# Kernel tuning notes

Measured on AMD Instinct MI355X. Metric: run time of the kernel, lower is better.

## Reference

```python
import jax, jax.numpy as jnp
from jax import lax
import numpy as np

KS = 8        # window size
SS = 4        # shift size = KS // 2
HEADS = 4


def _l2n(t, axis):
    # torch F.normalize: x / clamp(||x||_2, min=eps)
    return t / jnp.maximum(jnp.linalg.norm(t, axis=axis, keepdims=True), 1e-12)


def _to_windows(t, heads, ks):
    # 'b (head c) (h kh) (w kw) -> b head (h w) (kh kw) c'
    b, hc, H, W = t.shape
    c = hc // heads
    hW, wW = H // ks, W // ks
    t = t.reshape(b, heads, c, hW, ks, wW, ks)
    t = t.transpose(0, 1, 3, 5, 4, 6, 2)  # b,h,hW,wW,kh,kw,c
    return t.reshape(b, heads, hW * wW, ks * ks, c)


def _from_windows(t, hW, wW, ks):
    # 'b head (h w) (kh kw) c -> b (head c) (h kh) (w kw)'
    b, heads, nW, kk, c = t.shape
    t = t.reshape(b, heads, hW, wW, ks, ks, c)
    t = t.transpose(0, 1, 6, 2, 4, 3, 5)  # b,h,c,hW,kh,wW,kw
    return t.reshape(b, heads * c, hW * ks, wW * ks)


def _talk_conv(attn, w, hW, wW):
    # Conv3d(heads->heads, kernel (3,3,1), padding same) over the (hW, wW, K)
    # grid; kernel size 1 on K means an independent 2D conv per K slot, so we
    # fold K into the batch dim and run a single 2D conv.
    b, heads, nW, a1, a2 = attn.shape
    K = a1 * a2
    t = attn.reshape(b, heads, hW, wW, K).transpose(0, 4, 1, 2, 3)
    t = t.reshape(b * K, heads, hW, wW)
    t = lax.conv_general_dilated(t, w, (1, 1), 'SAME',
                                 dimension_numbers=('NCHW', 'OIHW', 'NCHW'))
    t = t.reshape(b, K, heads, hW, wW).transpose(0, 2, 3, 4, 1)
    return t.reshape(b, heads, nW, a1, a2)


def _shift_mask(H, W, ks, ss):
    # Swin-style shifted-window mask; pure numpy constant (shapes are static).
    img = np.zeros((H, W), np.float32)
    cnt = 0
    for hs in (slice(0, -ks), slice(-ks, -ss), slice(-ss, None)):
        for ws in (slice(0, -ks), slice(-ks, -ss), slice(-ss, None)):
            img[hs, ws] = cnt
            cnt += 1
    win = img.reshape(H // ks, ks, W // ks, ks).transpose(0, 2, 1, 3).reshape(-1, ks * ks)
    diff = win[:, None, :] - win[:, :, None]
    return jnp.asarray(np.where(diff != 0, -100.0, 0.0).astype(np.float32))


def _forward(x, w_quz, w_kv, temperature, r_talking, g_talking,
             b_talking_w, l_talking_w, dw_u_w, project_w, project_out_w,
             sca_w, sca_b):
    b, c, H, W = x.shape
    hW, wW = H // KS, W // KS
    quz = jnp.einsum('oc,bchw->bohw', w_quz, x)
    q, u, z = jnp.split(quz, 3, axis=1)
    kv = jnp.einsum('oc,bchw->bohw', w_kv, x)
    k, v = jnp.split(kv, 2, axis=1)
    # shift = True
    q, k, v = (jnp.roll(t, (-SS, -SS), axis=(-1, -2)) for t in (q, k, v))
    q, k, v = (_to_windows(t, HEADS, KS) for t in (q, k, v))  # b,h,nW,kk,c
    qb, ql, qg, qr = jnp.split(q, 4, axis=-1)
    kb, kl, kg, kr = jnp.split(k, 4, axis=-1)
    vb, vl, vg, vr = jnp.split(v, 4, axis=-1)
    qb, kb = _l2n(qb, -1), _l2n(kb, -1)
    ql, kl = _l2n(ql, -2), _l2n(kl, -2)
    qg, kg = _l2n(qg, -3), _l2n(kg, -3)
    qr, kr = _l2n(qr, -3), _l2n(kr, -3)
    # 4 branches (n=window index, i/j=position-in-window, c/d=per-branch chan)
    attn_b = jnp.einsum('bhnic,bhnjc->bhnij', qb, kb) * temperature[0]
    attn_l = jnp.einsum('bhnic,bhnid->bhncd', ql, kl) * temperature[1]
    attn_g = jnp.einsum('bhnic,bhnid->bhicd', qg, kg) * temperature[2]
    attn_r = jnp.einsum('bhnic,bhnjc->bhcij', qr, kr) * temperature[3]
    # talking heads
    attn_b = _talk_conv(attn_b, b_talking_w, hW, wW)
    attn_l = _talk_conv(attn_l, l_talking_w, hW, wW)
    attn_g = jnp.einsum('hklt,bhkcd->btlcd', g_talking, attn_g)
    attn_r = jnp.einsum('hcdt,bhcij->btdij', r_talking, attn_r)
    # shifted-window mask on the brightness branch
    attn_b = attn_b + _shift_mask(H, W, KS, SS)[None, None]
    attn_b, attn_l, attn_g, attn_r = (jax.nn.softmax(t, axis=-1)
                                      for t in (attn_b, attn_l, attn_g, attn_r))
    # outputs, all arranged to (b,h,n,i,c) before un-windowing
    out_b = jnp.einsum('bhnij,bhnjc->bhnic', attn_b, vb)
    out_l = jnp.einsum('bhncd,bhnid->bhnic', attn_l, vl)
    out_g = jnp.einsum('bhicd,bhnid->bhnic', attn_g, vg)
    out_r = jnp.einsum('bhcij,bhnjc->bhnic', attn_r, vr)
    out = jnp.concatenate([_from_windows(t, hW, wW, KS)
                           for t in (out_b, out_l, out_g, out_r)], axis=1)
    out = jnp.roll(out, (SS, SS), axis=(-1, -2))
    # simplified channel attention (global avg pool + 1x1 conv with bias)
    s = jnp.mean(out, axis=(2, 3))
    s = jnp.einsum('oc,bc->bo', sca_w, s) + sca_b
    out = jnp.einsum('oc,bchw->bohw', project_w, out * s[:, :, None, None])
    dw = lax.conv_general_dilated(u, dw_u_w, (1, 1), 'SAME',
                                  feature_group_count=u.shape[1],
                                  dimension_numbers=('NCHW', 'OIHW', 'NCHW'))
    out = out + dw
    return jnp.einsum('oc,bchw->bohw', project_out_w, out * z)


def setup_inputs() -> dict:
    key = jax.random.key(0)
    ks = jax.random.split(key, 12)
    dim, h_dim = 64, 128
    cd = h_dim // HEADS // 4
    b, H, W = 4, 192, 192
    r = lambda i, shp, s: jax.random.normal(ks[i], shp, jnp.float32) * s
    return {
        'x': jax.random.normal(ks[0], (b, dim, H, W), jnp.float32),
        'w_quz': r(1, (3 * h_dim, dim), 0.1),
        'w_kv': r(2, (2 * h_dim, dim), 0.1),
        'temperature': jnp.ones((4, HEADS, 1, 1, 1), jnp.float32),
        'r_talking': r(3, (HEADS, cd, cd, HEADS), 0.2),
        'g_talking': r(4, (HEADS, KS * KS, KS * KS, HEADS), 0.05),
        'b_talking_w': r(5, (HEADS, HEADS, 3, 3), 0.2),
        'l_talking_w': r(6, (HEADS, HEADS, 3, 3), 0.2),
        'dw_u_w': r(7, (h_dim, 1, 3, 3), 0.2),
        'project_w': r(8, (h_dim, h_dim), 0.08),
        'project_out_w': r(9, (dim, h_dim), 0.08),
        'sca_w': r(10, (h_dim, h_dim), 0.08),
        'sca_b': jnp.zeros((h_dim,), jnp.float32),
    }


def reference(x, w_quz, w_kv, temperature, r_talking, g_talking,
              b_talking_w, l_talking_w, dw_u_w, project_w, project_out_w,
              sca_w, sca_b):
    return _forward(x, w_quz, w_kv, temperature, r_talking, g_talking,
                    b_talking_w, l_talking_w, dw_u_w, project_w,
                    project_out_w, sca_w, sca_b)
```

## Files before the change

kernel.cpp:

```cpp
#include <hip/hip_runtime.h>
#include <cstdint>
#include <cstddef>

#define BB   4
#define CIN  64
#define HD   128
#define NH   4
#define CHW  32
#define CB   8
#define IMG  192
#define SSH  4
#define NWS  24
#define NWIN 576
#define KK   64
#define HWP  (IMG*IMG)

static const size_t NQK16  = (size_t)NH*NWIN*KK*16;
static const size_t NV32   = (size_t)NH*NWIN*KK*CHW;
static const size_t NGR    = (size_t)NH*KK*NWIN*CB;
static const size_t NSP    = (size_t)HD*HWP;
static const size_t NATTNB = (size_t)NH*NWIN*KK*KK;
static const size_t NATTNL = (size_t)NH*NWIN*64;
static const size_t NATTNG = (size_t)NH*KK*64;
static const size_t NATTNR = (size_t)NH*CB*KK*KK;
static const size_t NPART  = (size_t)8*NATTNR;

__device__ inline float wave_max(float v){
  #pragma unroll
  for (int s=1;s<64;s<<=1) v = fmaxf(v, __shfl_xor(v, s));
  return v;
}
__device__ inline float wave_sum(float v){
  #pragma unroll
  for (int s=1;s<64;s<<=1) v += __shfl_xor(v, s);
  return v;
}
__device__ inline float g8_max(float v){
  v = fmaxf(v, __shfl_xor(v,1)); v = fmaxf(v, __shfl_xor(v,2)); v = fmaxf(v, __shfl_xor(v,4));
  return v;
}
__device__ inline float g8_sum(float v){
  v += __shfl_xor(v,1); v += __shfl_xor(v,2); v += __shfl_xor(v,4);
  return v;
}
__device__ inline int regionc(int y){ return (y < IMG-8) ? 0 : ((y < IMG-4) ? 1 : 2); }

__device__ inline size_t widx(int h,int n,int i,int c){
  return (((size_t)h*NWIN + n)*KK + i)*CHW + c;
}
__device__ inline size_t widx16(int h,int n,int i,int c){
  return (((size_t)h*NWIN + n)*KK + i)*16 + c;
}
__device__ inline size_t gidx(int h,int i,int n,int c){
  return (((size_t)(h*KK + i))*NWIN + n)*CB + c;
}
__device__ inline size_t ridx(int h,int c,int n,int i){
  return (((size_t)(h*CB + c))*NWIN + n)*KK + i;
}

__global__ __launch_bounds__(256) void k1_proj(
    const float* __restrict__ x, const float* __restrict__ wquz, const float* __restrict__ wkv,
    float* __restrict__ qw, float* __restrict__ kw, float* __restrict__ vw,
    float* __restrict__ qg, float* __restrict__ kg,
    float* __restrict__ qr, float* __restrict__ kr,
    float* __restrict__ u, float* __restrict__ zbuf, int bsel)
{
  __shared__ float xs[64][16];
  int blk = blockIdx.x;
  int xc = blk % 12, y = blk / 12;
  int x0 = xc*16;
  int t = threadIdx.x;
  {
    int c = t >> 2, p4 = (t & 3)*4;
    float4 v = *(const float4*)&x[((size_t)(bsel*CIN+c)*IMG + y)*IMG + x0 + p4];
    *(float4*)&xs[c][p4] = v;
  }
  int py  = (y + IMG - SSH) % IMG;
  int kh  = py & 7, hwq = py >> 3;
  int wwA = ((x0 - SSH + IMG) % IMG) >> 3;
  int wwB = x0 >> 3;
  int wwC = (x0 + 8) >> 3;
  int pnA = hwq*NWS + wwA, pnB = hwq*NWS + wwB, pnC = hwq*NWS + wwC;
  int piA = kh*8 + 4, piB = kh*8, piC = kh*8;
  #define PN_(p) ((p)<4 ? pnA : ((p)<12 ? pnB : pnC))
  #define PI_(p) ((p)<4 ? (piA+(p)) : ((p)<12 ? (piB+(p)-4) : (piC+(p)-12)))
  __syncthreads();

  bool qkz = (t < 128);
  const float* wr1 = wquz + (size_t)t*CIN;
  const float* wr2 = wkv  + (size_t)t*CIN;

  float acc1[16], acc2[16], acc3[16];
  #pragma unroll
  for (int p = 0; p < 16; ++p){ acc1[p]=0.f; acc2[p]=0.f; acc3[p]=0.f; }

  if (qkz){
    const float* wr3 = wquz + (size_t)(t+256)*CIN;
    for (int cc4 = 0; cc4 < 64; cc4 += 4){
      float4 w1 = *(const float4*)(wr1+cc4);
      float4 w2 = *(const float4*)(wr2+cc4);
      float4 w3 = *(const float4*)(wr3+cc4);
      float w1a[4]={w1.x,w1.y,w1.z,w1.w};
      float w2a[4]={w2.x,w2.y,w2.z,w2.w};
      float w3a[4]={w3.x,w3.y,w3.z,w3.w};
      #pragma unroll
      for (int j = 0; j < 4; ++j){
        #pragma unroll
        for (int q = 0; q < 4; ++q){
          float4 xv = *(const float4*)&xs[cc4+j][q*4];
          acc1[q*4+0]+=w1a[j]*xv.x; acc1[q*4+1]+=w1a[j]*xv.y; acc1[q*4+2]+=w1a[j]*xv.z; acc1[q*4+3]+=w1a[j]*xv.w;
          acc2[q*4+0]+=w2a[j]*xv.x; acc2[q*4+1]+=w2a[j]*xv.y; acc2[q*4+2]+=w2a[j]*xv.z; acc2[q*4+3]+=w2a[j]*xv.w;
          acc3[q*4+0]+=w3a[j]*xv.x; acc3[q*4+1]+=w3a[j]*xv.y; acc3[q*4+2]+=w3a[j]*xv.z; acc3[q*4+3]+=w3a[j]*xv.w;
        }
      }
    }
    int h = t >> 5, c = t & 31;
    if (c < 16){
      #pragma unroll
      for (int p = 0; p < 16; ++p) qw[widx16(h,PN_(p),PI_(p),c)] = acc1[p];
      #pragma unroll
      for (int p = 0; p < 16; ++p) kw[widx16(h,PN_(p),PI_(p),c)] = acc2[p];
    } else if (c < 24){
      int cg = c - 16;
      #pragma unroll
      for (int p = 0; p < 16; ++p) qg[gidx(h,PI_(p),PN_(p),cg)] = acc1[p];
      #pragma unroll
      for (int p = 0; p < 16; ++p) kg[gidx(h,PI_(p),PN_(p),cg)] = acc2[p];
    } else {
      int cr = c - 24;
      *(float4*)&qr[ridx(h,cr,pnA,piA)]   = make_float4(acc1[0],acc1[1],acc1[2],acc1[3]);
      *(float4*)&qr[ridx(h,cr,pnB,piB)]   = make_float4(acc1[4],acc1[5],acc1[6],acc1[7]);
      *(float4*)&qr[ridx(h,cr,pnB,piB+4)] = make_float4(acc1[8],acc1[9],acc1[10],acc1[11]);
      *(float4*)&qr[ridx(h,cr,pnC,piC)]   = make_float4(acc1[12],acc1[13],acc1[14],acc1[15]);
      *(float4*)&kr[ridx(h,cr,pnA,piA)]   = make_float4(acc2[0],acc2[1],acc2[2],acc2[3]);
      *(float4*)&kr[ridx(h,cr,pnB,piB)]   = make_float4(acc2[4],acc2[5],acc2[6],acc2[7]);
      *(float4*)&kr[ridx(h,cr,pnB,piB+4)] = make_float4(acc2[8],acc2[9],acc2[10],acc2[11]);
      *(float4*)&kr[ridx(h,cr,pnC,piC)]   = make_float4(acc2[12],acc2[13],acc2[14],acc2[15]);
    }
    size_t zb = ((size_t)t*IMG + y)*IMG + x0;
    *(float4*)&zbuf[zb+ 0] = make_float4(acc3[0],acc3[1],acc3[2],acc3[3]);
    *(float4*)&zbuf[zb+ 4] = make_float4(acc3[4],acc3[5],acc3[6],acc3[7]);
    *(float4*)&zbuf[zb+ 8] = make_float4(acc3[8],acc3[9],acc3[10],acc3[11]);
    *(float4*)&zbuf[zb+12] = make_float4(acc3[12],acc3[13],acc3[14],acc3[15]);
  } else {
    for (int cc4 = 0; cc4 < 64; cc4 += 4){
      float4 w1 = *(const float4*)(wr1+cc4);
      float4 w2 = *(const float4*)(wr2+cc4);
      float w1a[4]={w1.x,w1.y,w1.z,w1.w};
      float w2a[4]={w2.x,w2.y,w2.z,w2.w};
      #pragma unroll
      for (int j = 0; j < 4; ++j){
        #pragma unroll
        for (int q = 0; q < 4; ++q){
          float4 xv = *(const float4*)&xs[cc4+j][q*4];
          acc1[q*4+0]+=w1a[j]*xv.x; acc1[q*4+1]+=w1a[j]*xv.y; acc1[q*4+2]+=w1a[j]*xv.z; acc1[q*4+3]+=w1a[j]*xv.w;
          acc2[q*4+0]+=w2a[j]*xv.x; acc2[q*4+1]+=w2a[j]*xv.y; acc2[q*4+2]+=w2a[j]*xv.z; acc2[q*4+3]+=w2a[j]*xv.w;
        }
      }
    }
    int ch = t - 128;
    size_t ub = ((size_t)ch*IMG + y)*IMG + x0;
    *(float4*)&u[ub+ 0] = make_float4(acc1[0],acc1[1],acc1[2],acc1[3]);
    *(float4*)&u[ub+ 4] = make_float4(acc1[4],acc1[5],acc1[6],acc1[7]);
    *(float4*)&u[ub+ 8] = make_float4(acc1[8],acc1[9],acc1[10],acc1[11]);
    *(float4*)&u[ub+12] = make_float4(acc1[12],acc1[13],acc1[14],acc1[15]);
    int h = ch >> 5, c = ch & 31;
    #pragma unroll
    for (int p = 0; p < 16; ++p) vw[widx(h,PN_(p),PI_(p),c)] = acc2[p];
  }
  #undef PN_
  #undef PI_
}

__global__ __launch_bounds__(256) void kA(
    const float* __restrict__ qw, const float* __restrict__ kw,
    const float* __restrict__ qg, const float* __restrict__ kg,
    const float* __restrict__ qr, const float* __restrict__ kr,
    const float* __restrict__ temp,
    float* __restrict__ attnB, float* __restrict__ attnL,
    float* __restrict__ attnG, float* __restrict__ part,
    float* __restrict__ invqr, float* __restrict__ invkr)
{
  __shared__ __align__(16) char smem[36864];
  int blk = blockIdx.x;
  int t = threadIdx.x;

  if (blk < 576){
    float (*qs)[64][8] = (float(*)[64][8])smem;
    int wv = t >> 6, j = t & 63;
    int gid = blk*4 + wv;
    int n = gid % NWIN, h = gid / NWIN;
    size_t base = widx16(h,n,j,0);
    float q8[CB], k8[CB];
    float sq = 0.f, sk2 = 0.f;
    #pragma unroll
    for (int c = 0; c < CB; ++c){
      q8[c] = qw[base+c]; sq += q8[c]*q8[c];
      k8[c] = kw[base+c]; sk2 += k8[c]*k8[c];
    }
    float invq = 1.f/fmaxf(sqrtf(sq),1e-12f), invk = 1.f/fmaxf(sqrtf(sk2),1e-12f);
    #pragma unroll
    for (int c = 0; c < CB; ++c){ qs[wv][j][c] = q8[c]*invq; k8[c] *= invk; }
    __syncthreads();
    float tmp = temp[h];
    float* orow = attnB + (size_t)gid*KK*KK;
    for (int i = 0; i < KK; ++i){
      float a = 0.f;
      #pragma unroll
      for (int c = 0; c < CB; ++c) a += qs[wv][i][c]*k8[c];
      orow[(size_t)i*KK + j] = a * tmp;
    }
  } else if (blk < 1152){
    int b2 = blk - 576;
    float (*qs)[64][8] = (float(*)[64][8])smem;
    float (*ks)[64][8] = (float(*)[64][8])(smem + 8192);
    float (*invqA)[8] = (float(*)[8])(smem + 16384);
    float (*invkA)[8] = (float(*)[8])(smem + 16384 + 128);
    int wv = t >> 6, tl = t & 63;
    int gid = b2*4 + wv;
    int n = gid % NWIN, h = gid / NWIN;
    size_t base = widx16(h,n,tl,8);
    #pragma unroll
    for (int c = 0; c < CB; ++c){ qs[wv][tl][c] = qw[base+c]; ks[wv][tl][c] = kw[base+c]; }
    __syncthreads();
    int c8 = tl & 7, ig = tl >> 3;
    float sq = 0.f, sk2 = 0.f;
    for (int i = ig; i < KK; i += 8){
      float a = qs[wv][i][c8]; sq += a*a;
      float b = ks[wv][i][c8]; sk2 += b*b;
    }
    #pragma unroll
    for (int m = 8; m < 64; m <<= 1){ sq += __shfl_xor(sq,m); sk2 += __shfl_xor(sk2,m); }
    if (tl < 8){ invqA[wv][tl] = 1.f/fmaxf(sqrtf(sq),1e-12f); invkA[wv][tl] = 1.f/fmaxf(sqrtf(sk2),1e-12f); }
    __syncthreads();
    int c = tl >> 3, d = tl & 7;
    float a = 0.f;
    for (int i = 0; i < KK; ++i) a += qs[wv][i][c]*ks[wv][i][d];
    attnL[(size_t)gid*64 + tl] = a * invqA[wv][c] * invkA[wv][d] * temp[NH + h];
  } else if (blk < 1408){
    int b2 = blk - 1152;
    int i = b2 & 63, h = b2 >> 6;
    float* sq = (float*)smem;
    float* sk = sq + 512;
    float (*redA)[64] = (float(*)[64])(smem + 4096);
    float (*redQ)[64] = (float(*)[64])(smem + 4096 + 1024);
    float (*redK)[64] = (float(*)[64])(smem + 4096 + 2048);
    size_t base = ((size_t)(h*KK+i))*NWIN*CB;
    int np = t >> 6, cd = t & 63, c = cd >> 3, d = cd & 7;
    float a = 0.f, qs2 = 0.f, ks2 = 0.f;
    for (int n0 = 0; n0 < NWIN; n0 += 64){
      __syncthreads();
      for (int idx = t; idx < 512; idx += 256){
        sq[idx] = qg[base + (size_t)n0*CB + idx];
        sk[idx] = kg[base + (size_t)n0*CB + idx];
      }
      __syncthreads();
      for (int nn = np; nn < 64; nn += 4){
        float qv = sq[nn*8+c], kv = sk[nn*8+d];
        a += qv*kv; qs2 += qv*qv; ks2 += kv*kv;
      }
    }
    __syncthreads();
    redA[np][cd] = a; redQ[np][cd] = qs2; redK[np][cd] = ks2;
    __syncthreads();
    if (t < 64){
      float at = redA[0][t]+redA[1][t]+redA[2][t]+redA[3][t];
      float qt = redQ[0][t]+redQ[1][t]+redQ[2][t]+redQ[3][t];
      float kt = redK[0][t]+redK[1][t]+redK[2][t]+redK[3][t];
      at *= (1.f/fmaxf(sqrtf(qt),1e-12f)) * (1.f/fmaxf(sqrtf(kt),1e-12f)) * temp[2*NH + h];
      attnG[(size_t)(h*KK+i)*64 + t] = at;
    }
  } else if (blk < 1664){
    int b2 = blk - 1408;
    int chunk = b2 >> 5, hc = b2 & 31;
    int n0 = chunk*72;
    float* sq = (float*)smem;
    float* sk = sq + 72*64;
    size_t base = (size_t)hc*NWIN*KK + (size_t)n0*KK;
    for (int idx = t; idx < 72*64/4; idx += 256){
      *(float4*)&sq[idx*4] = *(const float4*)&qr[base + (size_t)idx*4];
      *(float4*)&sk[idx*4] = *(const float4*)&kr[base + (size_t)idx*4];
    }
    __syncthreads();
    int j = t & 63, ig = t >> 6;
    float acc[16];
    #pragma unroll
    for (int p = 0; p < 16; ++p) acc[p] = 0.f;
    for (int nn = 0; nn < 72; ++nn){
      float kv = sk[nn*64+j];
      #pragma unroll
      for (int p = 0; p < 16; ++p) acc[p] += sq[nn*64 + ig*16 + p]*kv;
    }
    float* ob = part + (size_t)b2*4096;
    #pragma unroll
    for (int p = 0; p < 16; ++p) ob[(size_t)(ig*16+p)*64 + j] = acc[p];
  } else {
    int hc = blk - 1664;
    float (*rq)[64] = (float(*)[64])smem;
    float (*rk)[64] = (float(*)[64])(smem + 1024);
    size_t base = (size_t)hc*NWIN*KK;
    int i = t & 63, ng = t >> 6;
    float sq = 0.f, sk2 = 0.f;
    for (int n = ng; n < NWIN; n += 4){
      float a = qr[base + (size_t)n*KK + i]; sq  += a*a;
      float b = kr[base + (size_t)n*KK + i]; sk2 += b*b;
    }
    rq[ng][i] = sq; rk[ng][i] = sk2;
    __syncthreads();
    if (t < 64){
      float s = rq[0][t]+rq[1][t]+rq[2][t]+rq[3][t];
      invqr[hc*KK + t] = 1.f/fmaxf(sqrtf(s),1e-12f);
    } else if (t < 128){
      int i2 = t - 64;
      float s = rk[0][i2]+rk[1][i2]+rk[2][i2]+rk[3][i2];
      invkr[hc*KK + i2] = 1.f/fmaxf(sqrtf(s),1e-12f);
    }
  }
}

__global__ __launch_bounds__(256) void kB(
    const float* __restrict__ attnB, const float* __restrict__ btw,
    const float* __restrict__ vw, float* __restrict__ outa,
// ... 262 lines not shown
  __shared__ float red[256];
  red[threadIdx.x] = s; __syncthreads();
  for (int k = 128; k > 0; k >>= 1){
    if (threadIdx.x < k) red[threadIdx.x] += red[threadIdx.x + k];
    __syncthreads();
  }
  if (threadIdx.x == 0) meanb[ch] = red[0] / (float)HWP;
}

#define PADX 68
__global__ __launch_bounds__(256) void k9a(
    const float* __restrict__ outa, const float* __restrict__ meanb,
    const float* __restrict__ scaw, const float* __restrict__ scab,
    const float* __restrict__ projw, const float* __restrict__ dwu,
    const float* __restrict__ zbuf, float* __restrict__ out2z)
{
  __shared__ float WT[128][128];
  __shared__ float xsv[128][PADX];
  __shared__ float sv[128];
  int t = threadIdx.x;
  if (t < 128){
    float s = scab[t];
    const float* srow = scaw + (size_t)t*HD;
    for (int c = 0; c < HD; c += 4){
      float4 w = *(const float4*)&srow[c];
      float4 mm = *(const float4*)&meanb[c];
      s += w.x*mm.x + w.y*mm.y + w.z*mm.z + w.w*mm.w;
    }
    sv[t] = s;
  }
  for (int idx = t; idx < 4096; idx += 256){
    int o = idx & 127; int c4 = (idx >> 7) * 4;
    float4 w = *(const float4*)&projw[(size_t)o*HD + c4];
    WT[c4][o] = w.x; WT[c4+1][o] = w.y; WT[c4+2][o] = w.z; WT[c4+3][o] = w.w;
  }
  int px4 = (t & 15) * 4; int og8 = (t >> 4) * 8;
  for (int tile = 0; tile < 2; ++tile){
    int tid = blockIdx.x * 2 + tile;
    int y = tid / 3, x0 = (tid % 3) * 64;
    size_t sb = (size_t)y*IMG + x0;
    __syncthreads();
    for (int idx = t; idx < 2048; idx += 256){
      int c = idx >> 4; int p4 = (idx & 15) * 4;
      float4 v = *(const float4*)&outa[(size_t)c*HWP + sb + p4];
      float s = sv[c];
      xsv[c][p4] = v.x*s; xsv[c][p4+1] = v.y*s; xsv[c][p4+2] = v.z*s; xsv[c][p4+3] = v.w*s;
    }
    __syncthreads();
    float acc[8][4];
    #pragma unroll
    for (int a = 0; a < 8; ++a){ acc[a][0]=0.f; acc[a][1]=0.f; acc[a][2]=0.f; acc[a][3]=0.f; }
    for (int c = 0; c < 128; ++c){
      float4 xv = *(const float4*)&xsv[c][px4];
      float4 wA = *(const float4*)&WT[c][og8];
      float4 wB = *(const float4*)&WT[c][og8+4];
      float w8[8] = {wA.x,wA.y,wA.z,wA.w,wB.x,wB.y,wB.z,wB.w};
      #pragma unroll
      for (int a = 0; a < 8; ++a){
        acc[a][0] += w8[a]*xv.x; acc[a][1] += w8[a]*xv.y;
        acc[a][2] += w8[a]*xv.z; acc[a][3] += w8[a]*xv.w;
      }
    }
    #pragma unroll
    for (int oo = 0; oo < 8; ++oo){
      int o = og8 + oo;
      size_t off = (size_t)o*HWP + sb + px4;
      float4 d = *(const float4*)&dwu[off];
      float4 z = *(const float4*)&zbuf[off];
      float4 r;
      r.x = (acc[oo][0]+d.x)*z.x; r.y = (acc[oo][1]+d.y)*z.y;
      r.z = (acc[oo][2]+d.z)*z.z; r.w = (acc[oo][3]+d.w)*z.w;
      *(float4*)&out2z[off] = r;
    }
  }
}

__global__ __launch_bounds__(256) void k9b(
    const float* __restrict__ out2z, const float* __restrict__ projow,
    float* __restrict__ dout, int bsel)
{
  __shared__ float WT2[128][64];
  __shared__ float xsv[128][PADX];
  int t = threadIdx.x;
  for (int idx = t; idx < 2048; idx += 256){
    int o = idx & 63; int c4 = (idx >> 6) * 4;
    float4 w = *(const float4*)&projow[(size_t)o*HD + c4];
    WT2[c4][o] = w.x; WT2[c4+1][o] = w.y; WT2[c4+2][o] = w.z; WT2[c4+3][o] = w.w;
  }
  int px4 = (t & 15) * 4; int og4 = (t >> 4) * 4;
  for (int tile = 0; tile < 2; ++tile){
    int tid = blockIdx.x * 2 + tile;
    int y = tid / 3, x0 = (tid % 3) * 64;
    size_t sb = (size_t)y*IMG + x0;
    __syncthreads();
    for (int idx = t; idx < 2048; idx += 256){
      int c = idx >> 4; int p4 = (idx & 15) * 4;
      float4 v = *(const float4*)&out2z[(size_t)c*HWP + sb + p4];
      xsv[c][p4] = v.x; xsv[c][p4+1] = v.y; xsv[c][p4+2] = v.z; xsv[c][p4+3] = v.w;
    }
    __syncthreads();
    float acc[4][4];
    #pragma unroll
    for (int a = 0; a < 4; ++a){ acc[a][0]=0.f; acc[a][1]=0.f; acc[a][2]=0.f; acc[a][3]=0.f; }
    for (int c = 0; c < 128; ++c){
      float4 xv = *(const float4*)&xsv[c][px4];
      float4 w4 = *(const float4*)&WT2[c][og4];
      float w4a[4] = {w4.x,w4.y,w4.z,w4.w};
      #pragma unroll
      for (int a = 0; a < 4; ++a){
        acc[a][0] += w4a[a]*xv.x; acc[a][1] += w4a[a]*xv.y;
        acc[a][2] += w4a[a]*xv.z; acc[a][3] += w4a[a]*xv.w;
      }
    }
    #pragma unroll
    for (int oo = 0; oo < 4; ++oo){
      int o = og4 + oo;
      float4 r; r.x = acc[oo][0]; r.y = acc[oo][1]; r.z = acc[oo][2]; r.w = acc[oo][3];
      *(float4*)&dout[(size_t)(bsel*CIN + o)*HWP + sb + px4] = r;
    }
  }
}

extern "C" void kernel_launch(void* const* d_in, const int* in_sizes, int n_in,
                              void* d_out, int out_size, void* d_ws, size_t ws_size,
                              hipStream_t stream)
{
  const float* x     = (const float*)d_in[0];
  const float* wquz  = (const float*)d_in[1];
  const float* wkv   = (const float*)d_in[2];
  const float* temp  = (const float*)d_in[3];
  const float* rtalk = (const float*)d_in[4];
  const float* gtalk = (const float*)d_in[5];
  const float* btw   = (const float*)d_in[6];
  const float* ltw   = (const float*)d_in[7];
  const float* dww   = (const float*)d_in[8];
  const float* projw = (const float*)d_in[9];
  const float* projow= (const float*)d_in[10];
  const float* scaw  = (const float*)d_in[11];
  const float* scab  = (const float*)d_in[12];
  float* dout = (float*)d_out;

  float* ws = (float*)d_ws;
  float* qw    = ws;
  float* kw    = qw + NQK16;
  float* vw    = kw + NQK16;
  float* qg    = vw + NV32;
  float* kg    = qg + NGR;
  float* qr    = kg + NGR;
  float* kr    = qr + NGR;
  float* u     = kr + NGR;
  float* zbuf  = u + NSP;
  float* outa  = zbuf + NSP;
  float* attnB = outa + NSP;
  float* dwu   = attnB;
  float* out2z = attnB + NSP;
  float* attnL = attnB + NATTNB;
  float* attnG = attnL + NATTNL;
  float* attnGp= attnG + NATTNG;
  float* part  = attnGp + NATTNG;
  float* attnR = part + NPART;
  float* attnRp= attnR + NATTNR;
  float* invqr = attnRp + NATTNR;
  float* invkr = invqr + 2048;
  float* meanb = invkr + 2048;

  for (int b = 0; b < BB; ++b){
    k1_proj<<<IMG*12, 256, 0, stream>>>(x, wquz, wkv, qw, kw, vw, qg, kg, qr, kr, u, zbuf, b);

    kA<<<1696, 256, 0, stream>>>(qw, kw, qg, kg, qr, kr, temp,
                                 attnB, attnL, attnG, part, invqr, invkr);

    kB<<<16512, 256, 0, stream>>>(attnB, btw, vw, outa, attnL, ltw,
                                  attnG, gtalk, attnGp, part, invqr, invkr, temp, attnR,
                                  u, dww, out2z );

    kC<<<2336, 256, 0, stream>>>(attnGp, vw, outa, attnR, rtalk, attnRp);

    k7c<<<NH*NWIN, 256, 0, stream>>>(attnRp, vw, outa);

    k8_mean<<<HD, 256, 0, stream>>>(outa, meanb);

    k9a<<<288, 256, 0, stream>>>(outa, meanb, scaw, scab, projw, out2z , zbuf, dwu );
    k9b<<<288, 256, 0, stream>>>(dwu , projow, dout, b);
  }
}
```

Measured before the change: 1.471 ms.

## Rebalance projection kernel so every thread computes all five channel outputs

The projection kernel now processes 32-pixel rows per block. The two thread halves split the pixels, and each thread computes all five weight rows (q, k, z, u, v) for one channel over 16 pixels. Before, threads were split into uneven groups of three and two outputs. This removes warp divergence and load imbalance and halves the grid size, at the cost of more registers per thread (80 accumulators). Workspace aliasing for the dwu and out2z buffers is also remapped: kB's depthwise output moves into the qw region and the k9a/k9b argument roles are swapped.

```diff
diff --git a/kernel.cpp b/kernel.cpp
--- a/kernel.cpp
+++ b/kernel.cpp
@@ -65,109 +65,103 @@
     float* __restrict__ qr, float* __restrict__ kr,
     float* __restrict__ u, float* __restrict__ zbuf, int bsel)
 {
-  __shared__ float xs[64][16];
+  __shared__ float xs[64][32];
   int blk = blockIdx.x;
-  int xc = blk % 12, y = blk / 12;
-  int x0 = xc*16;
+  int xc = blk % 6, y = blk / 6;
+  int x0 = xc*32;
   int t = threadIdx.x;
   {
-    int c = t >> 2, p4 = (t & 3)*4;
-    float4 v = *(const float4*)&x[((size_t)(bsel*CIN+c)*IMG + y)*IMG + x0 + p4];
-    *(float4*)&xs[c][p4] = v;
-  }
+    int c = t >> 2, p8 = (t & 3)*8;
+    const float* xr = &x[((size_t)(bsel*CIN+c)*IMG + y)*IMG + x0 + p8];
+    *(float4*)&xs[c][p8]   = *(const float4*)xr;
+    *(float4*)&xs[c][p8+4] = *(const float4*)(xr+4);
+  }
+  int half = t >> 7, cp = t & 127;
+  int x0h = x0 + half*16;
   int py  = (y + IMG - SSH) % IMG;
   int kh  = py & 7, hwq = py >> 3;
-  int wwA = ((x0 - SSH + IMG) % IMG) >> 3;
-  int wwB = x0 >> 3;
-  int wwC = (x0 + 8) >> 3;
+  int wwA = ((x0h - SSH + IMG) % IMG) >> 3;
+  int wwB = x0h >> 3;
+  int wwC = (x0h + 8) >> 3;
   int pnA = hwq*NWS + wwA, pnB = hwq*NWS + wwB, pnC = hwq*NWS + wwC;
   int piA = kh*8 + 4, piB = kh*8, piC = kh*8;
   #define PN_(p) ((p)<4 ? pnA : ((p)<12 ? pnB : pnC))
   #define PI_(p) ((p)<4 ? (piA+(p)) : ((p)<12 ? (piB+(p)-4) : (piC+(p)-12)))
   __syncthreads();
 
-  bool qkz = (t < 128);
-  const float* wr1 = wquz + (size_t)t*CIN;
-  const float* wr2 = wkv  + (size_t)t*CIN;
-
-  float acc1[16], acc2[16], acc3[16];
+  const float* w0 = wquz + (size_t)cp*CIN;
+  const float* w1 = wkv  + (size_t)cp*CIN;
+  const float* w2 = wquz + (size_t)(cp+256)*CIN;
+  const float* w3 = wquz + (size_t)(cp+128)*CIN;
+  const float* w4 = wkv  + (size_t)(cp+128)*CIN;
+
+  float a0[16], a1[16], a2[16], a3[16], a4[16];
   #pragma unroll
-  for (int p = 0; p < 16; ++p){ acc1[p]=0.f; acc2[p]=0.f; acc3[p]=0.f; }
-
-  if (qkz){
-    const float* wr3 = wquz + (size_t)(t+256)*CIN;
-    for (int cc4 = 0; cc4 < 64; cc4 += 4){
-      float4 w1 = *(const float4*)(wr1+cc4);
-      float4 w2 = *(const float4*)(wr2+cc4);
-      float4 w3 = *(const float4*)(wr3+cc4);
-      float w1a[4]={w1.x,w1.y,w1.z,w1.w};
-      float w2a[4]={w2.x,w2.y,w2.z,w2.w};
-      float w3a[4]={w3.x,w3.y,w3.z,w3.w};
-      #pragma unroll
-      for (int j = 0; j < 4; ++j){
-        #pragma unroll
-        for (int q = 0; q < 4; ++q){
-          float4 xv = *(const float4*)&xs[cc4+j][q*4];
-          acc1[q*4+0]+=w1a[j]*xv.x; acc1[q*4+1]+=w1a[j]*xv.y; acc1[q*4+2]+=w1a[j]*xv.z; acc1[q*4+3]+=w1a[j]*xv.w;
-          acc2[q*4+0]+=w2a[j]*xv.x; acc2[q*4+1]+=w2a[j]*xv.y; acc2[q*4+2]+=w2a[j]*xv.z; acc2[q*4+3]+=w2a[j]*xv.w;
-          acc3[q*4+0]+=w3a[j]*xv.x; acc3[q*4+1]+=w3a[j]*xv.y; acc3[q*4+2]+=w3a[j]*xv.z; acc3[q*4+3]+=w3a[j]*xv.w;
-        }
-      }
-    }
-    int h = t >> 5, c = t & 31;
-    if (c < 16){
-      #pragma unroll
-      for (int p = 0; p < 16; ++p) qw[widx16(h,PN_(p),PI_(p),c)] = acc1[p];
-      #pragma unroll
-      for (int p = 0; p < 16; ++p) kw[widx16(h,PN_(p),PI_(p),c)] = acc2[p];
-    } else if (c < 24){
-      int cg = c - 16;
-      #pragma unroll
-      for (int p = 0; p < 16; ++p) qg[gidx(h,PI_(p),PN_(p),cg)] = acc1[p];
-      #pragma unroll
-      for (int p = 0; p < 16; ++p) kg[gidx(h,PI_(p),PN_(p),cg)] = acc2[p];
-    } else {
-      int cr = c - 24;
-      *(float4*)&qr[ridx(h,cr,pnA,piA)]   = make_float4(acc1[0],acc1[1],acc1[2],acc1[3]);
-      *(float4*)&qr[ridx(h,cr,pnB,piB)]   = make_float4(acc1[4],acc1[5],acc1[6],acc1[7]);
-      *(float4*)&qr[ridx(h,cr,pnB,piB+4)] = make_float4(acc1[8],acc1[9],acc1[10],acc1[11]);
-      *(float4*)&qr[ridx(h,cr,pnC,piC)]   = make_float4(acc1[12],acc1[13],acc1[14],acc1[15]);
-      *(float4*)&kr[ridx(h,cr,pnA,piA)]   = make_float4(acc2[0],acc2[1],acc2[2],acc2[3]);
-      *(float4*)&kr[ridx(h,cr,pnB,piB)]   = make_float4(acc2[4],acc2[5],acc2[6],acc2[7]);
-      *(float4*)&kr[ridx(h,cr,pnB,piB+4)] = make_float4(acc2[8],acc2[9],acc2[10],acc2[11]);
-      *(float4*)&kr[ridx(h,cr,pnC,piC)]   = make_float4(acc2[12],acc2[13],acc2[14],acc2[15]);
-    }
-    size_t zb = ((size_t)t*IMG + y)*IMG + x0;
-    *(float4*)&zbuf[zb+ 0] = make_float4(acc3[0],acc3[1],acc3[2],acc3[3]);
-    *(float4*)&zbuf[zb+ 4] = make_float4(acc3[4],acc3[5],acc3[6],acc3[7]);
-    *(float4*)&zbuf[zb+ 8] = make_float4(acc3[8],acc3[9],acc3[10],acc3[11]);
-    *(float4*)&zbuf[zb+12] = make_float4(acc3[12],acc3[13],acc3[14],acc3[15]);
+  for (int p = 0; p < 16; ++p){ a0[p]=0.f; a1[p]=0.f; a2[p]=0.f; a3[p]=0.f; a4[p]=0.f; }
+
+  int pb = half*16;
+  for (int cc4 = 0; cc4 < 64; cc4 += 4){
+    float4 W0 = *(const float4*)(w0+cc4);
+    float4 W1 = *(const float4*)(w1+cc4);
+    float4 W2 = *(const float4*)(w2+cc4);
+    float4 W3 = *(const float4*)(w3+cc4);
+    float4 W4 = *(const float4*)(w4+cc4);
+    float w0a[4]={W0.x,W0.y,W0.z,W0.w};
+    float w1a[4]={W1.x,W1.y,W1.z,W1.w};
+    float w2a[4]={W2.x,W2.y,W2.z,W2.w};
+    float w3a[4]={W3.x,W3.y,W3.z,W3.w};
+    float w4a[4]={W4.x,W4.y,W4.z,W4.w};
+    #pragma unroll
+    for (int j = 0; j < 4; ++j){
+      float f0=w0a[j], f1=w1a[j], f2=w2a[j], f3=w3a[j], f4=w4a[j];
+      #pragma unroll
+      for (int q = 0; q < 4; ++q){
+        float4 xv = *(const float4*)&xs[cc4+j][pb + q*4];
+        a0[q*4+0]+=f0*xv.x; a0[q*4+1]+=f0*xv.y; a0[q*4+2]+=f0*xv.z; a0[q*4+3]+=f0*xv.w;
+        a1[q*4+0]+=f1*xv.x; a1[q*4+1]+=f1*xv.y; a1[q*4+2]+=f1*xv.z; a1[q*4+3]+=f1*xv.w;
+        a2[q*4+0]+=f2*xv.x; a2[q*4+1]+=f2*xv.y; a2[q*4+2]+=f2*xv.z; a2[q*4+3]+=f2*xv.w;
+        a3[q*4+0]+=f3*xv.x; a3[q*4+1]+=f3*xv.y; a3[q*4+2]+=f3*xv.z; a3[q*4+3]+=f3*xv.w;
+        a4[q*4+0]+=f4*xv.x; a4[q*4+1]+=f4*xv.y; a4[q*4+2]+=f4*xv.z; a4[q*4+3]+=f4*xv.w;
+      }
+    }
+  }
+
+  int h = cp >> 5, c = cp & 31;
+  if (c < 16){
+    #pragma unroll
+    for (int p = 0; p < 16; ++p) qw[widx16(h,PN_(p),PI_(p),c)] = a0[p];
+    #pragma unroll
+    for (int p = 0; p < 16; ++p) kw[widx16(h,PN_(p),PI_(p),c)] = a1[p];
+  } else if (c < 24){
+    int cg = c - 16;
+    #pragma unroll
+    for (int p = 0; p < 16; ++p) qg[gidx(h,PI_(p),PN_(p),cg)] = a0[p];
+    #pragma unroll
+    for (int p = 0; p < 16; ++p) kg[gidx(h,PI_(p),PN_(p),cg)] = a1[p];
   } else {
-    for (int cc4 = 0; cc4 < 64; cc4 += 4){
-      float4 w1 = *(const float4*)(wr1+cc4);
-      float4 w2 = *(const float4*)(wr2+cc4);
-      float w1a[4]={w1.x,w1.y,w1.z,w1.w};
-      float w2a[4]={w2.x,w2.y,w2.z,w2.w};
-      #pragma unroll
-      for (int j = 0; j < 4; ++j){
-        #pragma unroll
-        for (int q = 0; q < 4; ++q){
-          float4 xv = *(const float4*)&xs[cc4+j][q*4];
-          acc1[q*4+0]+=w1a[j]*xv.x; acc1[q*4+1]+=w1a[j]*xv.y; acc1[q*4+2]+=w1a[j]*xv.z; acc1[q*4+3]+=w1a[j]*xv.w;
-          acc2[q*4+0]+=w2a[j]*xv.x; acc2[q*4+1]+=w2a[j]*xv.y; acc2[q*4+2]+=w2a[j]*xv.z; acc2[q*4+3]+=w2a[j]*xv.w;
-        }
-      }
-    }
-    int ch = t - 128;
-    size_t ub = ((size_t)ch*IMG + y)*IMG + x0;
-    *(float4*)&u[ub+ 0] = make_float4(acc1[0],acc1[1],acc1[2],acc1[3]);
-    *(float4*)&u[ub+ 4] = make_float4(acc1[4],acc1[5],acc1[6],acc1[7]);
-    *(float4*)&u[ub+ 8] = make_float4(acc1[8],acc1[9],acc1[10],acc1[11]);
-    *(float4*)&u[ub+12] = make_float4(acc1[12],acc1[13],acc1[14],acc1[15]);
-    int h = ch >> 5, c = ch & 31;
-    #pragma unroll
-    for (int p = 0; p < 16; ++p) vw[widx(h,PN_(p),PI_(p),c)] = acc2[p];
-  }
+    int cr = c - 24;
+    *(float4*)&qr[ridx(h,cr,pnA,piA)]   = make_float4(a0[0],a0[1],a0[2],a0[3]);
+    *(float4*)&qr[ridx(h,cr,pnB,piB)]   = make_float4(a0[4],a0[5],a0[6],a0[7]);
+    *(float4*)&qr[ridx(h,cr,pnB,piB+4)] = make_float4(a0[8],a0[9],a0[10],a0[11]);
+    *(float4*)&qr[ridx(h,cr,pnC,piC)]   = make_float4(a0[12],a0[13],a0[14],a0[15]);
+    *(float4*)&kr[ridx(h,cr,pnA,piA)]   = make_float4(a1[0],a1[1],a1[2],a1[3]);
+    *(float4*)&kr[ridx(h,cr,pnB,piB)]   = make_float4(a1[4],a1[5],a1[6],a1[7]);
+    *(float4*)&kr[ridx(h,cr,pnB,piB+4)] = make_float4(a1[8],a1[9],a1[10],a1[11]);
+    *(float4*)&kr[ridx(h,cr,pnC,piC)]   = make_float4(a1[12],a1[13],a1[14],a1[15]);
+  }
+  {
+    size_t zb = ((size_t)cp*IMG + y)*IMG + x0h;
+    *(float4*)&zbuf[zb+ 0] = make_float4(a2[0],a2[1],a2[2],a2[3]);
+    *(float4*)&zbuf[zb+ 4] = make_float4(a2[4],a2[5],a2[6],a2[7]);
+    *(float4*)&zbuf[zb+ 8] = make_float4(a2[8],a2[9],a2[10],a2[11]);
+    *(float4*)&zbuf[zb+12] = make_float4(a2[12],a2[13],a2[14],a2[15]);
+    *(float4*)&u[zb+ 0] = make_float4(a3[0],a3[1],a3[2],a3[3]);
+    *(float4*)&u[zb+ 4] = make_float4(a3[4],a3[5],a3[6],a3[7]);
+    *(float4*)&u[zb+ 8] = make_float4(a3[8],a3[9],a3[10],a3[11]);
+    *(float4*)&u[zb+12] = make_float4(a3[12],a3[13],a3[14],a3[15]);
+  }
+  #pragma unroll
+  for (int p = 0; p < 16; ++p) vw[widx(h,PN_(p),PI_(p),c)] = a4[p];
   #undef PN_
   #undef PI_
 }
@@ -736,8 +730,6 @@
   float* zbuf  = u + NSP;
   float* outa  = zbuf + NSP;
   float* attnB = outa + NSP;
-  float* dwu   = attnB;
-  float* out2z = attnB + NSP;
   float* attnL = attnB + NATTNB;
   float* attnG = attnL + NATTNL;
   float* attnGp= attnG + NATTNG;
@@ -747,16 +739,18 @@
   float* invqr = attnRp + NATTNR;
   float* invkr = invqr + 2048;
   float* meanb = invkr + 2048;
+  float* dwu   = qw;
+  float* out2z = attnB;
 
   for (int b = 0; b < BB; ++b){
-    k1_proj<<<IMG*12, 256, 0, stream>>>(x, wquz, wkv, qw, kw, vw, qg, kg, qr, kr, u, zbuf, b);
+    k1_proj<<<IMG*6, 256, 0, stream>>>(x, wquz, wkv, qw, kw, vw, qg, kg, qr, kr, u, zbuf, b);
 
     kA<<<1696, 256, 0, stream>>>(qw, kw, qg, kg, qr, kr, temp,
                                  attnB, attnL, attnG, part, invqr, invkr);
 
     kB<<<16512, 256, 0, stream>>>(attnB, btw, vw, outa, attnL, ltw,
                                   attnG, gtalk, attnGp, part, invqr, invkr, temp, attnR,
-                                  u, dww, out2z );
+                                  u, dww, dwu);
 
     kC<<<2336, 256, 0, stream>>>(attnGp, vw, outa, attnR, rtalk, attnRp);
 
@@ -764,7 +758,7 @@
 
     k8_mean<<<HD, 256, 0, stream>>>(outa, meanb);
 
-    k9a<<<288, 256, 0, stream>>>(outa, meanb, scaw, scab, projw, out2z , zbuf, dwu );
-    k9b<<<288, 256, 0, stream>>>(dwu , projow, dout, b);
-  }
-}
+    k9a<<<288, 256, 0, stream>>>(outa, meanb, scaw, scab, projw, dwu, zbuf, out2z);
+    k9b<<<288, 256, 0, stream>>>(out2z, projow, dout, b);
+  }
+}
```

Result: no change. 1.478 ms (+0.4%).

## Rebalance projection work across threads and remap workspace buffer aliases

Applied to the files above, without the earlier changes.

Reworks k1_proj so every thread computes two 16-pixel output rows (q/k-family or u/v) and then half of a z row, replacing the old split where half the threads carried three accumulator sets. This evens the per-thread load and cuts register pressure. The shared tile row is padded from 16 to 20 floats to change the LDS bank mapping. The workspace aliases for dwu and out2z are also reassigned (dwu now reuses the qw region, out2z the attnB region), and the kB/k9a/k9b arguments are swapped to match. The aliasing depends on qw/attnB being dead at those points, which risks a correctness hazard.

```diff
diff --git a/kernel.cpp b/kernel.cpp
--- a/kernel.cpp
+++ b/kernel.cpp
@@ -65,7 +65,7 @@
     float* __restrict__ qr, float* __restrict__ kr,
     float* __restrict__ u, float* __restrict__ zbuf, int bsel)
 {
-  __shared__ float xs[64][16];
+  __shared__ float xs[64][20];
   int blk = blockIdx.x;
   int xc = blk % 12, y = blk / 12;
   int x0 = xc*16;
@@ -86,87 +86,77 @@
   #define PI_(p) ((p)<4 ? (piA+(p)) : ((p)<12 ? (piB+(p)-4) : (piC+(p)-12)))
   __syncthreads();
 
-  bool qkz = (t < 128);
-  const float* wr1 = wquz + (size_t)t*CIN;
-  const float* wr2 = wkv  + (size_t)t*CIN;
-
-  float acc1[16], acc2[16], acc3[16];
-  #pragma unroll
-  for (int p = 0; p < 16; ++p){ acc1[p]=0.f; acc2[p]=0.f; acc3[p]=0.f; }
-
-  if (qkz){
-    const float* wr3 = wquz + (size_t)(t+256)*CIN;
-    for (int cc4 = 0; cc4 < 64; cc4 += 4){
-      float4 w1 = *(const float4*)(wr1+cc4);
-      float4 w2 = *(const float4*)(wr2+cc4);
-      float4 w3 = *(const float4*)(wr3+cc4);
-      float w1a[4]={w1.x,w1.y,w1.z,w1.w};
-      float w2a[4]={w2.x,w2.y,w2.z,w2.w};
-      float w3a[4]={w3.x,w3.y,w3.z,w3.w};
-      #pragma unroll
-      for (int j = 0; j < 4; ++j){
-        #pragma unroll
-        for (int q = 0; q < 4; ++q){
-          float4 xv = *(const float4*)&xs[cc4+j][q*4];
-          acc1[q*4+0]+=w1a[j]*xv.x; acc1[q*4+1]+=w1a[j]*xv.y; acc1[q*4+2]+=w1a[j]*xv.z; acc1[q*4+3]+=w1a[j]*xv.w;
-          acc2[q*4+0]+=w2a[j]*xv.x; acc2[q*4+1]+=w2a[j]*xv.y; acc2[q*4+2]+=w2a[j]*xv.z; acc2[q*4+3]+=w2a[j]*xv.w;
-          acc3[q*4+0]+=w3a[j]*xv.x; acc3[q*4+1]+=w3a[j]*xv.y; acc3[q*4+2]+=w3a[j]*xv.z; acc3[q*4+3]+=w3a[j]*xv.w;
-        }
-      }
-    }
-    int h = t >> 5, c = t & 31;
-    if (c < 16){
-      #pragma unroll
-      for (int p = 0; p < 16; ++p) qw[widx16(h,PN_(p),PI_(p),c)] = acc1[p];
-      #pragma unroll
-      for (int p = 0; p < 16; ++p) kw[widx16(h,PN_(p),PI_(p),c)] = acc2[p];
-    } else if (c < 24){
-      int cg = c - 16;
-      #pragma unroll
-      for (int p = 0; p < 16; ++p) qg[gidx(h,PI_(p),PN_(p),cg)] = acc1[p];
-      #pragma unroll
-      for (int p = 0; p < 16; ++p) kg[gidx(h,PI_(p),PN_(p),cg)] = acc2[p];
+  int o;
+  if (t < 64)       o = (t>>4)*32 + (t&15);
+  else if (t < 96)  o = ((t-64)>>3)*32 + 16 + (t&7);
+  else if (t < 128) o = ((t-96)>>3)*32 + 24 + (t&7);
+  else              o = t;
+
+  for (int oi = 0; oi < 2; ++oi){
+    const float* wr = (oi == 0) ? (wquz + (size_t)o*CIN) : (wkv + (size_t)o*CIN);
+    float acc[16];
+    #pragma unroll
+    for (int p = 0; p < 16; ++p) acc[p] = 0.f;
+    for (int cc = 0; cc < 64; cc += 4){
+      float4 w4 = *(const float4*)(wr + cc);
+      #pragma unroll
+      for (int p = 0; p < 16; ++p){
+        acc[p] += w4.x * xs[cc  ][p];
+        acc[p] += w4.y * xs[cc+1][p];
+        acc[p] += w4.z * xs[cc+2][p];
+        acc[p] += w4.w * xs[cc+3][p];
+      }
+    }
+    if (t < 64){
+      float* dst = (oi == 0) ? qw : kw;
+      int h = t >> 4, c = t & 15;
+      #pragma unroll
+      for (int p = 0; p < 16; ++p) dst[widx16(h,PN_(p),PI_(p),c)] = acc[p];
+    } else if (t < 96){
+      float* dst = (oi == 0) ? qg : kg;
+      int h = (t-64) >> 3, cg = t & 7;
+      #pragma unroll
+      for (int p = 0; p < 16; ++p) dst[gidx(h,PI_(p),PN_(p),cg)] = acc[p];
+    } else if (t < 128){
+      float* dst = (oi == 0) ? qr : kr;
+      int h = (t-96) >> 3, cr = t & 7;
+      *(float4*)&dst[ridx(h,cr,pnA,piA)]   = make_float4(acc[0],acc[1],acc[2],acc[3]);
+      *(float4*)&dst[ridx(h,cr,pnB,piB)]   = make_float4(acc[4],acc[5],acc[6],acc[7]);
+      *(float4*)&dst[ridx(h,cr,pnB,piB+4)] = make_float4(acc[8],acc[9],acc[10],acc[11]);
+      *(float4*)&dst[ridx(h,cr,pnC,piC)]   = make_float4(acc[12],acc[13],acc[14],acc[15]);
+    } else if (oi == 0){
+      size_t ub = ((size_t)(o-128)*IMG + y)*IMG + x0;
+      *(float4*)&u[ub+ 0] = make_float4(acc[0],acc[1],acc[2],acc[3]);
+      *(float4*)&u[ub+ 4] = make_float4(acc[4],acc[5],acc[6],acc[7]);
+      *(float4*)&u[ub+ 8] = make_float4(acc[8],acc[9],acc[10],acc[11]);
+      *(float4*)&u[ub+12] = make_float4(acc[12],acc[13],acc[14],acc[15]);
     } else {
-      int cr = c - 24;
-      *(float4*)&qr[ridx(h,cr,pnA,piA)]   = make_float4(acc1[0],acc1[1],acc1[2],acc1[3]);
-      *(float4*)&qr[ridx(h,cr,pnB,piB)]   = make_float4(acc1[4],acc1[5],acc1[6],acc1[7]);
-      *(float4*)&qr[ridx(h,cr,pnB,piB+4)] = make_float4(acc1[8],acc1[9],acc1[10],acc1[11]);
-      *(float4*)&qr[ridx(h,cr,pnC,piC)]   = make_float4(acc1[12],acc1[13],acc1[14],acc1[15]);
-      *(float4*)&kr[ridx(h,cr,pnA,piA)]   = make_float4(acc2[0],acc2[1],acc2[2],acc2[3]);
-      *(float4*)&kr[ridx(h,cr,pnB,piB)]   = make_float4(acc2[4],acc2[5],acc2[6],acc2[7]);
-      *(float4*)&kr[ridx(h,cr,pnB,piB+4)] = make_float4(acc2[8],acc2[9],acc2[10],acc2[11]);
-      *(float4*)&kr[ridx(h,cr,pnC,piC)]   = make_float4(acc2[12],acc2[13],acc2[14],acc2[15]);
-    }
-    size_t zb = ((size_t)t*IMG + y)*IMG + x0;
-    *(float4*)&zbuf[zb+ 0] = make_float4(acc3[0],acc3[1],acc3[2],acc3[3]);
-    *(float4*)&zbuf[zb+ 4] = make_float4(acc3[4],acc3[5],acc3[6],acc3[7]);
-    *(float4*)&zbuf[zb+ 8] = make_float4(acc3[8],acc3[9],acc3[10],acc3[11]);
-    *(float4*)&zbuf[zb+12] = make_float4(acc3[12],acc3[13],acc3[14],acc3[15]);
-  } else {
-    for (int cc4 = 0; cc4 < 64; cc4 += 4){
-      float4 w1 = *(const float4*)(wr1+cc4);
-      float4 w2 = *(const float4*)(wr2+cc4);
-      float w1a[4]={w1.x,w1.y,w1.z,w1.w};
-      float w2a[4]={w2.x,w2.y,w2.z,w2.w};
-      #pragma unroll
-      for (int j = 0; j < 4; ++j){
-        #pragma unroll
-        for (int q = 0; q < 4; ++q){
-          float4 xv = *(const float4*)&xs[cc4+j][q*4];
-          acc1[q*4+0]+=w1a[j]*xv.x; acc1[q*4+1]+=w1a[j]*xv.y; acc1[q*4+2]+=w1a[j]*xv.z; acc1[q*4+3]+=w1a[j]*xv.w;
-          acc2[q*4+0]+=w2a[j]*xv.x; acc2[q*4+1]+=w2a[j]*xv.y; acc2[q*4+2]+=w2a[j]*xv.z; acc2[q*4+3]+=w2a[j]*xv.w;
-        }
-      }
-    }
-    int ch = t - 128;
-    size_t ub = ((size_t)ch*IMG + y)*IMG + x0;
-    *(float4*)&u[ub+ 0] = make_float4(acc1[0],acc1[1],acc1[2],acc1[3]);
-    *(float4*)&u[ub+ 4] = make_float4(acc1[4],acc1[5],acc1[6],acc1[7]);
-    *(float4*)&u[ub+ 8] = make_float4(acc1[8],acc1[9],acc1[10],acc1[11]);
-    *(float4*)&u[ub+12] = make_float4(acc1[12],acc1[13],acc1[14],acc1[15]);
-    int h = ch >> 5, c = ch & 31;
-    #pragma unroll
-    for (int p = 0; p < 16; ++p) vw[widx(h,PN_(p),PI_(p),c)] = acc2[p];
+      int oc = o - 128; int h = oc >> 5, c = oc & 31;
+      #pragma unroll
+      for (int p = 0; p < 16; ++p) vw[widx(h,PN_(p),PI_(p),c)] = acc[p];
+    }
+  }
+
+  {
+    int zr = t >> 1, ph = t & 1;
+    const float* wr = wquz + (size_t)(256 + zr)*CIN;
+    int pb = ph*8;
+    float acc[8];
+    #pragma unroll
+    for (int p = 0; p < 8; ++p) acc[p] = 0.f;
+    for (int cc = 0; cc < 64; cc += 4){
+      float4 w4 = *(const float4*)(wr + cc);
+      #pragma unroll
+      for (int p = 0; p < 8; ++p){
+        acc[p] += w4.x * xs[cc  ][pb+p];
+        acc[p] += w4.y * xs[cc+1][pb+p];
+        acc[p] += w4.z * xs[cc+2][pb+p];
+        acc[p] += w4.w * xs[cc+3][pb+p];
+      }
+    }
+    size_t zb = ((size_t)zr*IMG + y)*IMG + x0 + pb;
+    *(float4*)&zbuf[zb]   = make_float4(acc[0],acc[1],acc[2],acc[3]);
+    *(float4*)&zbuf[zb+4] = make_float4(acc[4],acc[5],acc[6],acc[7]);
   }
   #undef PN_
   #undef PI_
@@ -736,8 +726,6 @@
   float* zbuf  = u + NSP;
   float* outa  = zbuf + NSP;
   float* attnB = outa + NSP;
-  float* dwu   = attnB;
-  float* out2z = attnB + NSP;
   float* attnL = attnB + NATTNB;
   float* attnG = attnL + NATTNL;
   float* attnGp= attnG + NATTNG;
@@ -747,6 +735,8 @@
   float* invqr = attnRp + NATTNR;
   float* invkr = invqr + 2048;
   float* meanb = invkr + 2048;
+  float* dwu   = qw;
+  float* out2z = attnB;
 
   for (int b = 0; b < BB; ++b){
     k1_proj<<<IMG*12, 256, 0, stream>>>(x, wquz, wkv, qw, kw, vw, qg, kg, qr, kr, u, zbuf, b);
@@ -756,7 +746,7 @@
 
     kB<<<16512, 256, 0, stream>>>(attnB, btw, vw, outa, attnL, ltw,
                                   attnG, gtalk, attnGp, part, invqr, invkr, temp, attnR,
-                                  u, dww, out2z );
+                                  u, dww, dwu);
 
     kC<<<2336, 256, 0, stream>>>(attnGp, vw, outa, attnR, rtalk, attnRp);
 
@@ -764,7 +754,7 @@
 
     k8_mean<<<HD, 256, 0, stream>>>(outa, meanb);
 
-    k9a<<<288, 256, 0, stream>>>(outa, meanb, scaw, scab, projw, out2z , zbuf, dwu );
-    k9b<<<288, 256, 0, stream>>>(dwu , projow, dout, b);
-  }
-}
+    k9a<<<288, 256, 0, stream>>>(outa, meanb, scaw, scab, projw, dwu, zbuf, out2z);
+    k9b<<<288, 256, 0, stream>>>(out2z, projow, dout, b);
+  }
+}
```

New measurement: 1.356 ms. 1.09x faster.
